# Performance work log

Hardware: AMD Instinct MI355X
Metric: run time of the kernel (lower is better)

## Reference

```python
import jax, jax.numpy as jnp
import numpy as np

D = 1024      # input_dim / embed_dim
H = 1024      # hidden_dim
H2 = H // 2
M = 15        # n_masks
NH = 4        # n_heads
B = 8192
LN_EPS = 1e-5


def setup_inputs() -> dict:
    key = jax.random.key(0)
    ks = jax.random.split(key, 16)
    s = 0.02
    return {
        "x": jax.random.normal(ks[0], (B, D), jnp.float32),
        # nn.MultiheadAttention params (torch layout: y = x @ W.T + b)
        "in_proj_w": jax.random.normal(ks[1], (3 * D, D), jnp.float32) * s,
        "in_proj_b": jax.random.normal(ks[2], (3 * D,), jnp.float32) * s,
        "out_proj_w": jax.random.normal(ks[3], (D, D), jnp.float32) * s,
        "out_proj_b": jax.random.normal(ks[4], (D,), jnp.float32) * s,
        # 15 mask MLPs stacked along leading axis (grouped GEMM form)
        "W1": jax.random.normal(ks[5], (M, D, H), jnp.float32) * s,
        "b1": jax.random.normal(ks[6], (M, H), jnp.float32) * s,
        "ln_g": jnp.ones((M, H), jnp.float32),
        "ln_b": jnp.zeros((M, H), jnp.float32),
        "W2": jax.random.normal(ks[7], (M, H, H2), jnp.float32) * s,
        "b2": jax.random.normal(ks[8], (M, H2), jnp.float32) * s,
        "W3": jax.random.normal(ks[9], (M, H2, D), jnp.float32) * s,
        "b3": jax.random.normal(ks[10], (M, D), jnp.float32) * s,
    }


def reference(x, in_proj_w, in_proj_b, out_proj_w, out_proj_b,
              W1, b1, ln_g, ln_b, W2, b2, W3, b3):
    Bn = x.shape[0]
    hd = D // NH
    # --- seq_len=1 self-attention ---
    qkv = x @ in_proj_w.T + in_proj_b                      # [B, 3D]
    q, k, v = jnp.split(qkv, 3, axis=-1)                   # each [B, D]
    qh = q.reshape(Bn, NH, hd)
    kh = k.reshape(Bn, NH, hd)
    vh = v.reshape(Bn, NH, hd)
    scores = jnp.sum(qh * kh, axis=-1) / jnp.sqrt(jnp.float32(hd))  # [B, NH]
    # softmax over kv length = 1 -> all ones (kept for faithfulness)
    w = jax.nn.softmax(scores[..., None], axis=-1)         # [B, NH, 1]
    attn = (w * vh).reshape(Bn, D)                         # [B, D]
    a = attn @ out_proj_w.T + out_proj_b                   # [B, D]
    # --- 15 mask MLPs as one grouped GEMM stack (Dropout is eval->identity) ---
    h1 = jnp.einsum('bd,mdh->mbh', a, W1) + b1[:, None, :]  # [M, B, H]
    mu = jnp.mean(h1, axis=-1, keepdims=True)
    var = jnp.mean(jnp.square(h1 - mu), axis=-1, keepdims=True)
    h1 = (h1 - mu) * jax.lax.rsqrt(var + LN_EPS) * ln_g[:, None, :] + ln_b[:, None, :]
    h1 = jax.nn.gelu(h1, approximate=False)
    h2 = jnp.einsum('mbh,mhk->mbk', h1, W2) + b2[:, None, :]  # [M, B, H2]
    h2 = jax.nn.gelu(h2, approximate=False)
    h3 = jnp.einsum('mbk,mkd->mbd', h2, W3) + b3[:, None, :]  # [M, B, D]
    return jax.nn.sigmoid(h3)                               # [M, B, D]
```

## Files before the change

### kernel.cpp

```cpp
#include <hip/hip_runtime.h>

#define D_  1024
#define H_  1024
#define H2_ 512
#define M_  15
#define B_  8192

typedef __attribute__((ext_vector_type(4))) float f32x4;
typedef __attribute__((ext_vector_type(8))) short short8;

__device__ __forceinline__ unsigned short f2bf(float f) {
  unsigned int u = __float_as_uint(f);
  u += 0x7fffu + ((u >> 16) & 1u);
  return (unsigned short)(u >> 16);
}
__device__ __forceinline__ float bf2f(unsigned int h) {
  return __uint_as_float(h << 16);
}
__device__ __forceinline__ float gelu_exact(float x) {
  return 0.5f * x * (1.0f + erff(x * 0.70710678118654752440f));
}

__global__ void cast_f32_bf16(const float* __restrict__ in, unsigned short* __restrict__ out, int n4) {
  int i = blockIdx.x * blockDim.x + threadIdx.x;
  if (i >= n4) return;
  float4 v = ((const float4*)in)[i];
  ushort4 o;
  o.x = f2bf(v.x); o.y = f2bf(v.y); o.z = f2bf(v.z); o.w = f2bf(v.w);
  ((ushort4*)out)[i] = o;
}

__global__ void transpose_cast(const float* __restrict__ in, unsigned short* __restrict__ out,
                               int K, int N) {
  __shared__ float t[32][33];
  const size_t mo = (size_t)blockIdx.z * K * N;
  in  += mo;
  out += mo;
  const int k0 = blockIdx.x * 32, n0 = blockIdx.y * 32;
  const int tx = threadIdx.x, ty = threadIdx.y;
#pragma unroll
  for (int j = 0; j < 32; j += 8)
    t[ty + j][tx] = in[(size_t)(k0 + ty + j) * N + (n0 + tx)];
  __syncthreads();
#pragma unroll
  for (int j = 0; j < 32; j += 8)
    out[(size_t)(n0 + ty + j) * K + (k0 + tx)] = f2bf(t[tx][ty + j]);
}

template <int EPI>
__launch_bounds__(256, 3)
__global__ void gemm_bt(const unsigned short* __restrict__ A, const unsigned short* __restrict__ Bt,
                        const float* __restrict__ bias, void* __restrict__ Cout,
                        int Mrows, int N, int K,
                        long sA, long sB, long sBias, long sC) {
  __shared__ __align__(16) unsigned short As[128 * 64];
  __shared__ __align__(16) unsigned short Bs[128 * 64];
  const int mz = blockIdx.z;
  A    += (size_t)mz * sA;
  Bt   += (size_t)mz * sB;
  bias += (size_t)mz * sBias;

  const int tid  = threadIdx.x;
  const int w    = tid >> 6;
  const int lane = tid & 63;
  const int row0 = blockIdx.x * 128;
  const int col0 = blockIdx.y * 128;

  f32x4 acc[4][4];
#pragma unroll
  for (int i = 0; i < 4; ++i)
#pragma unroll
    for (int j = 0; j < 4; ++j) acc[i][j] = (f32x4){0.f, 0.f, 0.f, 0.f};

  const int wm = w >> 1, wn = w & 1;
  const int mrow = lane & 15;
  const int kq   = (lane >> 4) << 3;

  for (int k0 = 0; k0 < K; k0 += 64) {
    __syncthreads();
#pragma unroll
    for (int i = 0; i < 4; ++i) {
      const int c  = i * 256 + tid;
      const int m  = c >> 3;
      const int kk = (c & 7) << 3;
      const unsigned short* gA = A  + (size_t)(row0 + m) * K + (k0 + kk);
      const unsigned short* gB = Bt + (size_t)(col0 + m) * K + (k0 + kk);
      const int ldsoff = (i * 256 + w * 64) * 8;
      __builtin_amdgcn_global_load_lds((const __attribute__((address_space(1))) void*)gA,
                                       (__attribute__((address_space(3))) void*)(As + ldsoff),
                                       16, 0, 0);
      __builtin_amdgcn_global_load_lds((const __attribute__((address_space(1))) void*)gB,
                                       (__attribute__((address_space(3))) void*)(Bs + ldsoff),
                                       16, 0, 0);
    }
    __syncthreads();
#pragma unroll
    for (int ki = 0; ki < 64; ki += 32) {
      short8 af[4], bf[4];
#pragma unroll
      for (int f = 0; f < 4; ++f) {
        af[f] = *(const short8*)(As + (wm * 64 + f * 16 + mrow) * 64 + ki + kq);
        bf[f] = *(const short8*)(Bs + (wn * 64 + f * 16 + mrow) * 64 + ki + kq);
      }
#pragma unroll
      for (int fm = 0; fm < 4; ++fm)
#pragma unroll
        for (int fn = 0; fn < 4; ++fn)
          acc[fm][fn] = __builtin_amdgcn_mfma_f32_16x16x32_bf16(af[fm], bf[fn], acc[fm][fn], 0, 0, 0);
    }
  }

  float*          Cf = (float*)Cout          + (size_t)mz * sC;
  unsigned short* Cb = (unsigned short*)Cout + (size_t)mz * sC;
  const int rq = (lane >> 4) << 2;
  const int cl = lane & 15;
#pragma unroll
  for (int fm = 0; fm < 4; ++fm) {
#pragma unroll
    for (int fn = 0; fn < 4; ++fn) {
      const int cc = col0 + wn * 64 + fn * 16 + cl;
      const float bv = bias[cc];
#pragma unroll
      for (int r = 0; r < 4; ++r) {
        const int rr = row0 + wm * 64 + fm * 16 + rq + r;
        float v = acc[fm][fn][r] + bv;
        if (EPI == 2) {
          Cf[(size_t)rr * N + cc] = 1.0f / (1.0f + __expf(-v));
        } else {
          if (EPI == 1) v = gelu_exact(v);
          Cb[(size_t)rr * N + cc] = f2bf(v);
        }
      }
    }
  }
}

#define BAR()   asm volatile("s_barrier" ::: "memory")
#define LGKM0() asm volatile("s_waitcnt lgkmcnt(0)" ::: "memory")
#define VM6()   asm volatile("s_waitcnt vmcnt(6)" ::: "memory")

#define STG_A(bufi, kt, rho0) do {                                                             \
  _Pragma("unroll")                                                                            \
  for (int j_ = 0; j_ < 2; ++j_) {                                                             \
    const int rho_ = (rho0) + j_ * 64 + (tid >> 3);                                            \
    const int gr_  = (((rho_ >> 6) & 1) << 7) | (((rho_ >> 7) & 1) << 6) | (rho_ & 63);        \
    const unsigned short* g_ = A + (size_t)(row0 + gr_) * K + (size_t)(kt) * 64                \
                                 + (((tid & 7) ^ (rho_ & 7)) << 3);                            \
    __builtin_amdgcn_global_load_lds((const __attribute__((address_space(1))) void*)g_,        \
        (__attribute__((address_space(3))) void*)(&As[bufi][(rho0) * 64 + (j_ * 512 + w6 * 64) * 8]), \
        16, 0, 0);                                                                             \
  }                                                                                            \
} while (0)

#define STG_B(bufi, kt, rho0) do {                                                             \
  _Pragma("unroll")                                                                            \
  for (int j_ = 0; j_ < 2; ++j_) {                                                             \
    const int rho_ = (rho0) + j_ * 64 + (tid >> 3);                                            \
    const int gc_  = (((rho_ >> 5) & 3) << 6) | (((rho_ >> 7) & 1) << 5) | (rho_ & 31);        \
    const unsigned short* g_ = Bt + (size_t)(col0 + gc_) * K + (size_t)(kt) * 64               \
                                  + (((tid & 7) ^ (rho_ & 7)) << 3);                           \
    __builtin_amdgcn_global_load_lds((const __attribute__((address_space(1))) void*)g_,        \
        (__attribute__((address_space(3))) void*)(&Bs[bufi][(rho0) * 64 + (j_ * 512 + w6 * 64) * 8]), \
        16, 0, 0);                                                                             \
  }                                                                                            \
} while (0)

#define LDA4(bufi, hi) do {                                                                    \
  _Pragma("unroll")                                                                            \
  for (int q_ = 0; q_ < 4; ++q_) {                                                             \
    const int rho_ = ((hi) ? 128 : 0) + wm * 64 + q_ * 16 + lrow;                              \
    a[q_][0] = *(const short8*)&As[bufi][rho_ * 64 + ((lk ^ (rho_ & 7)) << 3)];                \
    a[q_][1] = *(const short8*)&As[bufi][rho_ * 64 + (((4 + lk) ^ (rho_ & 7)) << 3)];          \
  }                                                                                            \
} while (0)

#define LDB2(bufi, hi) do {                                                                    \
  _Pragma("unroll")                                                                            \
  for (int q_ = 0; q_ < 2; ++q_) {                                                             \
    const int rho_ = ((hi) ? 128 : 0) + wn * 32 + q_ * 16 + lrow;                              \
    b[(hi) * 2 + q_][0] = *(const short8*)&Bs[bufi][rho_ * 64 + ((lk ^ (rho_ & 7)) << 3)];     \
    b[(hi) * 2 + q_][1] = *(const short8*)&Bs[bufi][rho_ * 64 + (((4 + lk) ^ (rho_ & 7)) << 3)]; \
  }                                                                                            \
} while (0)

#define MMQ(mh, nh) do {                                                                       \
  __builtin_amdgcn_s_setprio(1);                                                               \
  _Pragma("unroll")                                                                            \
  for (int mq_ = 0; mq_ < 4; ++mq_) {                                                          \
    _Pragma("unroll")                                                                          \
    for (int nq_ = 0; nq_ < 2; ++nq_) {                                                        \
      acc[(mh) * 4 + mq_][(nh) * 2 + nq_] = __builtin_amdgcn_mfma_f32_16x16x32_bf16(           \
          a[mq_][0], b[(nh) * 2 + nq_][0], acc[(mh) * 4 + mq_][(nh) * 2 + nq_], 0, 0, 0);      \
      acc[(mh) * 4 + mq_][(nh) * 2 + nq_] = __builtin_amdgcn_mfma_f32_16x16x32_bf16(           \
          a[mq_][1], b[(nh) * 2 + nq_][1], acc[(mh) * 4 + mq_][(nh) * 2 + nq_], 0, 0, 0);      \
    }                                                                                          \
  }                                                                                            \
  __builtin_amdgcn_s_setprio(0);                                                               \
} while (0)

template <int EPI>
__launch_bounds__(512, 2)
__global__ void gemm256(const unsigned short* __restrict__ A, const unsigned short* __restrict__ Bt,
                        const float* __restrict__ bias, void* __restrict__ Cout,
                        int N, int K, long sA, long sB, long sBias, long sC) {
  __shared__ __align__(16) unsigned short As[2][256 * 64];
  __shared__ __align__(16) unsigned short Bs[2][256 * 64];

  const int gx = gridDim.x, gy = gridDim.y;
  const int nwg = gx * gy * gridDim.z;
  const int bid = blockIdx.x + gx * (blockIdx.y + gy * blockIdx.z);
  int orig = bid;
  if ((nwg & 7) == 0) {
    const int cpx = nwg >> 3;
    orig = (bid & 7) * cpx + (bid >> 3);
  }
  const int bx = orig % gx;
  const int r1 = orig / gx;
  const int by = r1 % gy;
  const int mz = r1 / gy;

  A    += (size_t)mz * sA;
  Bt   += (size_t)mz * sB;
  bias += (size_t)mz * sBias;

  const int tid  = threadIdx.x;
  const int w6   = tid >> 6;
  const int lane = tid & 63;
  const int wm   = w6 >> 2;
  const int wn   = w6 & 3;
  const int lrow = lane & 15;
  const int lk   = lane >> 4;
  const int row0 = bx * 256;
  const int col0 = by * 256;
  const int nt   = K >> 6;

  f32x4 acc[8][4];
#pragma unroll
  for (int i = 0; i < 8; ++i)
#pragma unroll
    for (int j = 0; j < 4; ++j) acc[i][j] = (f32x4){0.f, 0.f, 0.f, 0.f};
  short8 a[4][2], b[4][2];

  STG_A(0, 0, 0); STG_B(0, 0, 0); STG_B(0, 0, 128); STG_A(0, 0, 128);
  STG_A(1, 1, 0); STG_B(1, 1, 0); STG_B(1, 1, 128);
  VM6(); BAR();

#pragma unroll 1
  for (int it = 0; it < (nt >> 1); ++it) {
    const int T  = it * 2;
    const int t2 = (T + 2 < nt) ? T + 2 : nt - 1;
    const int t3 = (T + 3 < nt) ? T + 3 : nt - 1;
    LDA4(0, 0); LDB2(0, 0);
    STG_A(1, T + 1, 128);
    BAR(); LGKM0();
    MMQ(0, 0);
    BAR();
    LDB2(0, 1);
    STG_A(0, t2, 0);
    BAR(); LGKM0();
    MMQ(0, 1);
    BAR();
    LDA4(0, 1);
    STG_B(0, t2, 0);
    BAR(); LGKM0();
    MMQ(1, 0);
    BAR();
    STG_B(0, t2, 128);
    VM6(); BAR();
    MMQ(1, 1);
    BAR();
    LDA4(1, 0); LDB2(1, 0);
    STG_A(0, t2, 128);
    BAR(); LGKM0();
    MMQ(0, 0);
    BAR();
    LDB2(1, 1);
    STG_A(1, t3, 0);
    BAR(); LGKM0();
    MMQ(0, 1);
    BAR();
    LDA4(1, 1);
    STG_B(1, t3, 0);
    BAR(); LGKM0();
    MMQ(1, 0);
    BAR();
    STG_B(1, t3, 128);
    VM6(); BAR();
    MMQ(1, 1);
    BAR();
  }
  asm volatile("s_waitcnt vmcnt(0)" ::: "memory");

  float*          Cf = (float*)Cout          + (size_t)mz * sC;
  unsigned short* Cb = (unsigned short*)Cout + (size_t)mz * sC;
  const int rq = (lane >> 4) << 2;
  const int cl = lane & 15;
#pragma unroll
  for (int nf = 0; nf < 4; ++nf) {
    const int cc = col0 + wn * 64 + nf * 16 + cl;
    const float bv = bias[cc];
#pragma unroll
    for (int mf = 0; mf < 8; ++mf) {
#pragma unroll
      for (int r = 0; r < 4; ++r) {
        const int rr = row0 + wm * 128 + mf * 16 + rq + r;
        float v = acc[mf][nf][r] + bv;
        if (EPI == 2) {
          Cf[(size_t)rr * N + cc] = 1.0f / (1.0f + __expf(-v));
        } else {
          if (EPI == 1) v = gelu_exact(v);
          Cb[(size_t)rr * N + cc] = f2bf(v);
        }
      }
    }
  }
}

__global__ void ln_gelu(const unsigned short* __restrict__ in, const float* __restrict__ g,
                        const float* __restrict__ bb, unsigned short* __restrict__ out) {
  const int m = blockIdx.y;
  in  += (size_t)m * B_ * H_;
  out += (size_t)m * B_ * H_;
  g   += (size_t)m * H_;
  bb  += (size_t)m * H_;
  const int row = blockIdx.x;
  const int tid = threadIdx.x;
  const unsigned short* rp = in + (size_t)row * H_;
  uint2 u = ((const uint2*)rp)[tid];
  float x0 = bf2f(u.x & 0xffffu);
  float x1 = bf2f(u.x >> 16);
  float x2 = bf2f(u.y & 0xffffu);
  float x3 = bf2f(u.y >> 16);

  float s  = x0 + x1 + x2 + x3;
  float s2 = x0 * x0 + x1 * x1 + x2 * x2 + x3 * x3;
#pragma unroll
  for (int o = 32; o > 0; o >>= 1) {
    s  += __shfl_down(s, o);
    s2 += __shfl_down(s2, o);
  }
  __shared__ float red[10];
  const int w = tid >> 6;
  if ((tid & 63) == 0) { red[w] = s; red[4 + w] = s2; }
  __syncthreads();
  if (tid == 0) {
    float ts = red[0] + red[1] + red[2] + red[3];
    float t2 = red[4] + red[5] + red[6] + red[7];
    float mean = ts * (1.0f / H_);
    float var  = t2 * (1.0f / H_) - mean * mean;
    red[8] = mean;
    red[9] = rsqrtf(var + 1e-5f);
  }
  __syncthreads();
  const float mean = red[8], rstd = red[9];
  const int col = tid * 4;
  float y0 = gelu_exact((x0 - mean) * rstd * g[col + 0] + bb[col + 0]);
  float y1 = gelu_exact((x1 - mean) * rstd * g[col + 1] + bb[col + 1]);
  float y2 = gelu_exact((x2 - mean) * rstd * g[col + 2] + bb[col + 2]);
  float y3 = gelu_exact((x3 - mean) * rstd * g[col + 3] + bb[col + 3]);
  ushort4 o;
  o.x = f2bf(y0); o.y = f2bf(y1); o.z = f2bf(y2); o.w = f2bf(y3);
  ((ushort4*)(out + (size_t)row * H_))[tid] = o;
}

extern "C" void kernel_launch(void* const* d_in, const int* in_sizes, int n_in,
                              void* d_out, int out_size, void* d_ws, size_t ws_size,
                              hipStream_t stream) {
  const float* x   = (const float*)d_in[0];
  const float* ipw = (const float*)d_in[1];
  const float* ipb = (const float*)d_in[2];
  const float* opw = (const float*)d_in[3];
  const float* opb = (const float*)d_in[4];
  const float* W1  = (const float*)d_in[5];
  const float* b1  = (const float*)d_in[6];
  const float* lng = (const float*)d_in[7];
  const float* lnb = (const float*)d_in[8];
  const float* W2  = (const float*)d_in[9];
  const float* b2  = (const float*)d_in[10];
  const float* W3  = (const float*)d_in[11];
  const float* b3  = (const float*)d_in[12];
  float* out = (float*)d_out;

  char* p = (char*)d_ws;
  auto take = [&](size_t bytes) { void* q = (void*)p; p += (bytes + 255) & ~(size_t)255; return q; };
  unsigned short* xb  = (unsigned short*)take((size_t)B_ * D_ * 2);
  unsigned short* wvb = (unsigned short*)take((size_t)D_ * D_ * 2);
  unsigned short* wob = (unsigned short*)take((size_t)D_ * D_ * 2);
  unsigned short* w1t = (unsigned short*)take((size_t)M_ * H_ * D_ * 2);
  unsigned short* w2t = (unsigned short*)take((size_t)M_ * H2_ * H_ * 2);
  unsigned short* w3t = (unsigned short*)take((size_t)M_ * D_ * H2_ * 2);
  unsigned short* vb  = (unsigned short*)take((size_t)B_ * D_ * 2);
  unsigned short* ab  = (unsigned short*)take((size_t)B_ * D_ * 2);
  unsigned short* h1p = (unsigned short*)take((size_t)M_ * B_ * H_ * 2);
  unsigned short* h1a = (unsigned short*)take((size_t)M_ * B_ * H_ * 2);
  unsigned short* h2b = (unsigned short*)take((size_t)M_ * B_ * H2_ * 2);

  cast_f32_bf16<<<dim3((B_ * D_ / 4 + 255) / 256), 256, 0, stream>>>(x, xb, B_ * D_ / 4);
  cast_f32_bf16<<<dim3((D_ * D_ / 4 + 255) / 256), 256, 0, stream>>>(ipw + 2 * D_ * D_, wvb, D_ * D_ / 4);
  cast_f32_bf16<<<dim3((D_ * D_ / 4 + 255) / 256), 256, 0, stream>>>(opw, wob, D_ * D_ / 4);
  transpose_cast<<<dim3(D_ / 32, H_ / 32, M_), dim3(32, 8), 0, stream>>>(W1, w1t, D_, H_);
  transpose_cast<<<dim3(H_ / 32, H2_ / 32, M_), dim3(32, 8), 0, stream>>>(W2, w2t, H_, H2_);
  transpose_cast<<<dim3(H2_ / 32, D_ / 32, M_), dim3(32, 8), 0, stream>>>(W3, w3t, H2_, D_);

  gemm_bt<0><<<dim3(B_ / 128, D_ / 128, 1), 256, 0, stream>>>(
      xb, wvb, ipb + 2 * D_, vb, B_, D_, D_, 0, 0, 0, 0);
  gemm_bt<0><<<dim3(B_ / 128, D_ / 128, 1), 256, 0, stream>>>(
      vb, wob, opb, ab, B_, D_, D_, 0, 0, 0, 0);

  gemm256<0><<<dim3(B_ / 256, H_ / 256, M_), 512, 0, stream>>>(
      ab, w1t, b1, h1p, H_, D_,
      0, (long)H_ * D_, (long)H_, (long)B_ * H_);
  ln_gelu<<<dim3(B_, M_), 256, 0, stream>>>(h1p, lng, lnb, h1a);
  gemm256<1><<<dim3(B_ / 256, H2_ / 256, M_), 512, 0, stream>>>(
      h1a, w2t, b2, h2b, H2_, H_,
      (long)B_ * H_, (long)H2_ * H_, (long)H2_, (long)B_ * H2_);
  gemm256<2><<<dim3(B_ / 256, D_ / 256, M_), 512, 0, stream>>>(
      h2b, w3t, b3, out, D_, H2_,
      (long)B_ * H2_, (long)D_ * H2_, (long)D_, (long)B_ * D_);
}
```

Baseline: 1.731 ms.

## Make grouped GEMMs persistent with cross-tile prefetch over a fixed grid

Replaces the per-tile launch of the three grouped MLP GEMMs with a persistent kernel of 240 workgroups. Each workgroup walks several output tiles in sequence, and the K-loop prefetch runs across tile boundaries, so loads for the next tile overlap the current tile's tail and epilogue. This is meant to remove the wave-quantization tail and the per-tile pipeline fill and drain. In exchange the epilogue now sits inside the main loop, which adds register pressure and per-iteration address arithmetic. The hard-coded tile stride of 30 and the XCD mapping depend on the grid size.

Result: faster. 1.623 ms (-6.2%).

```diff
diff --git a/kernel.cpp b/kernel.cpp
--- a/kernel.cpp
+++ b/kernel.cpp
@@ -139,26 +139,24 @@
 #define LGKM0() asm volatile("s_waitcnt lgkmcnt(0)" ::: "memory")
 #define VM6()   asm volatile("s_waitcnt vmcnt(6)" ::: "memory")
 
-#define STG_A(bufi, kt, rho0) do {                                                             \
+#define STG_A(bufi, bA, rho0) do {                                                             \
   _Pragma("unroll")                                                                            \
   for (int j_ = 0; j_ < 2; ++j_) {                                                             \
     const int rho_ = (rho0) + j_ * 64 + (tid >> 3);                                            \
     const int gr_  = (((rho_ >> 6) & 1) << 7) | (((rho_ >> 7) & 1) << 6) | (rho_ & 63);        \
-    const unsigned short* g_ = A + (size_t)(row0 + gr_) * K + (size_t)(kt) * 64                \
-                                 + (((tid & 7) ^ (rho_ & 7)) << 3);                            \
+    const unsigned short* g_ = (bA) + (size_t)gr_ * K + (((tid & 7) ^ (rho_ & 7)) << 3);       \
     __builtin_amdgcn_global_load_lds((const __attribute__((address_space(1))) void*)g_,        \
         (__attribute__((address_space(3))) void*)(&As[bufi][(rho0) * 64 + (j_ * 512 + w6 * 64) * 8]), \
         16, 0, 0);                                                                             \
   }                                                                                            \
 } while (0)
 
-#define STG_B(bufi, kt, rho0) do {                                                             \
+#define STG_B(bufi, bB, rho0) do {                                                             \
   _Pragma("unroll")                                                                            \
   for (int j_ = 0; j_ < 2; ++j_) {                                                             \
     const int rho_ = (rho0) + j_ * 64 + (tid >> 3);                                            \
     const int gc_  = (((rho_ >> 5) & 3) << 6) | (((rho_ >> 7) & 1) << 5) | (rho_ & 31);        \
-    const unsigned short* g_ = Bt + (size_t)(col0 + gc_) * K + (size_t)(kt) * 64               \
-                                  + (((tid & 7) ^ (rho_ & 7)) << 3);                           \
+    const unsigned short* g_ = (bB) + (size_t)gc_ * K + (((tid & 7) ^ (rho_ & 7)) << 3);       \
     __builtin_amdgcn_global_load_lds((const __attribute__((address_space(1))) void*)g_,        \
         (__attribute__((address_space(3))) void*)(&Bs[bufi][(rho0) * 64 + (j_ * 512 + w6 * 64) * 8]), \
         16, 0, 0);                                                                             \
@@ -198,30 +196,19 @@
   __builtin_amdgcn_s_setprio(0);                                                               \
 } while (0)
 
-template <int EPI>
+template <int EPI, int LNT, int LGY>
 __launch_bounds__(512, 2)
-__global__ void gemm256(const unsigned short* __restrict__ A, const unsigned short* __restrict__ Bt,
-                        const float* __restrict__ bias, void* __restrict__ Cout,
-                        int N, int K, long sA, long sB, long sBias, long sC) {
+__global__ void gemm256p(const unsigned short* __restrict__ A, const unsigned short* __restrict__ Bt,
+                         const float* __restrict__ bias, void* __restrict__ Cout,
+                         int N, int K, long sA, long sB, long sBias, long sC,
+                         int ntiles8, int tpb) {
   __shared__ __align__(16) unsigned short As[2][256 * 64];
   __shared__ __align__(16) unsigned short Bs[2][256 * 64];
-
-  const int gx = gridDim.x, gy = gridDim.y;
-  const int nwg = gx * gy * gridDim.z;
-  const int bid = blockIdx.x + gx * (blockIdx.y + gy * blockIdx.z);
-  int orig = bid;
-  if ((nwg & 7) == 0) {
-    const int cpx = nwg >> 3;
-    orig = (bid & 7) * cpx + (bid >> 3);
-  }
-  const int bx = orig % gx;
-  const int r1 = orig / gx;
-  const int by = r1 % gy;
-  const int mz = r1 / gy;
-
-  A    += (size_t)mz * sA;
-  Bt   += (size_t)mz * sB;
-  bias += (size_t)mz * sBias;
+  const int NT = 1 << LNT, GYm1 = (1 << LGY) - 1;
+
+  const int bid = blockIdx.x;
+  const int xcd = bid & 7, lb = bid >> 3;
+  const int cb  = xcd * ntiles8;
 
   const int tid  = threadIdx.x;
   const int w6   = tid >> 6;
@@ -230,9 +217,14 @@
   const int wn   = w6 & 3;
   const int lrow = lane & 15;
   const int lk   = lane >> 4;
-  const int row0 = bx * 256;
-  const int col0 = by * 256;
-  const int nt   = K >> 6;
+
+  int t_cur = 0;
+  int tix  = cb + lb;
+  int row0 = ((tix >> LGY) & 31) << 8;
+  int col0 = (tix & GYm1) << 8;
+  int mz   = tix >> (LGY + 5);
+  const unsigned short* bAc = A  + (size_t)mz * sA + (size_t)row0 * K;
+  const unsigned short* bBc = Bt + (size_t)mz * sB + (size_t)col0 * K;
 
   f32x4 acc[8][4];
 #pragma unroll
@@ -241,79 +233,92 @@
     for (int j = 0; j < 4; ++j) acc[i][j] = (f32x4){0.f, 0.f, 0.f, 0.f};
   short8 a[4][2], b[4][2];
 
-  STG_A(0, 0, 0); STG_B(0, 0, 0); STG_B(0, 0, 128); STG_A(0, 0, 128);
-  STG_A(1, 1, 0); STG_B(1, 1, 0); STG_B(1, 1, 128);
+  STG_A(0, bAc, 0); STG_B(0, bBc, 0); STG_B(0, bBc, 128); STG_A(0, bAc, 128);
+  STG_A(1, bAc + 64, 0); STG_B(1, bBc + 64, 0); STG_B(1, bBc + 64, 128);
   VM6(); BAR();
 
+  const int totK = tpb << LNT;
 #pragma unroll 1
-  for (int it = 0; it < (nt >> 1); ++it) {
-    const int T  = it * 2;
-    const int t2 = (T + 2 < nt) ? T + 2 : nt - 1;
-    const int t3 = (T + 3 < nt) ? T + 3 : nt - 1;
+  for (int T = 0; T < totK; T += 2) {
+    const int g2 = (T + 2 < totK) ? T + 2 : totK - 1;
+    const int g3 = (T + 3 < totK) ? T + 3 : totK - 1;
+    const int t2 = g2 >> LNT, t3 = g3 >> LNT;
+    const int tix2 = cb + lb + t2 * 30;
+    const int tix3 = cb + lb + t3 * 30;
+    const unsigned short* bA2 = A  + (size_t)(tix2 >> (LGY + 5)) * sA
+                                   + (size_t)((((tix2 >> LGY) & 31) << 8)) * K + ((g2 & (NT - 1)) << 6);
+    const unsigned short* bB2 = Bt + (size_t)(tix2 >> (LGY + 5)) * sB
+                                   + (size_t)(((tix2 & GYm1) << 8)) * K + ((g2 & (NT - 1)) << 6);
+    const unsigned short* bA3 = A  + (size_t)(tix3 >> (LGY + 5)) * sA
+                                   + (size_t)((((tix3 >> LGY) & 31) << 8)) * K + ((g3 & (NT - 1)) << 6);
+    const unsigned short* bB3 = Bt + (size_t)(tix3 >> (LGY + 5)) * sB
+                                   + (size_t)(((tix3 & GYm1) << 8)) * K + ((g3 & (NT - 1)) << 6);
+    const unsigned short* bA1 = bAc + (((T + 1) & (NT - 1)) << 6);
+
     LDA4(0, 0); LDB2(0, 0);
-    STG_A(1, T + 1, 128);
-    BAR(); LGKM0();
-    MMQ(0, 0);
-    BAR();
+    STG_A(1, bA1, 128);
+    BAR(); LGKM0(); MMQ(0, 0); BAR();
     LDB2(0, 1);
-    STG_A(0, t2, 0);
-    BAR(); LGKM0();
-    MMQ(0, 1);
-    BAR();
+    STG_A(0, bA2, 0);
+    BAR(); LGKM0(); MMQ(0, 1); BAR();
     LDA4(0, 1);
-    STG_B(0, t2, 0);
-    BAR(); LGKM0();
-    MMQ(1, 0);
-    BAR();
-    STG_B(0, t2, 128);
-    VM6(); BAR();
-    MMQ(1, 1);
-    BAR();
+    STG_B(0, bB2, 0);
+    BAR(); LGKM0(); MMQ(1, 0); BAR();
+    STG_B(0, bB2, 128);
+    VM6(); BAR(); MMQ(1, 1); BAR();
     LDA4(1, 0); LDB2(1, 0);
-    STG_A(0, t2, 128);
-    BAR(); LGKM0();
-    MMQ(0, 0);
-    BAR();
+    STG_A(0, bA2, 128);
+    BAR(); LGKM0(); MMQ(0, 0); BAR();
     LDB2(1, 1);
-    STG_A(1, t3, 0);
-    BAR(); LGKM0();
-    MMQ(0, 1);
-    BAR();
+    STG_A(1, bA3, 0);
+    BAR(); LGKM0(); MMQ(0, 1); BAR();
     LDA4(1, 1);
-    STG_B(1, t3, 0);
-    BAR(); LGKM0();
-    MMQ(1, 0);
-    BAR();
-    STG_B(1, t3, 128);
-    VM6(); BAR();
-    MMQ(1, 1);
-    BAR();
-  }
-  asm volatile("s_waitcnt vmcnt(0)" ::: "memory");
-
-  float*          Cf = (float*)Cout          + (size_t)mz * sC;
-  unsigned short* Cb = (unsigned short*)Cout + (size_t)mz * sC;
-  const int rq = (lane >> 4) << 2;
-  const int cl = lane & 15;
-#pragma unroll
-  for (int nf = 0; nf < 4; ++nf) {
-    const int cc = col0 + wn * 64 + nf * 16 + cl;
-    const float bv = bias[cc];
-#pragma unroll
-    for (int mf = 0; mf < 8; ++mf) {
-#pragma unroll
-      for (int r = 0; r < 4; ++r) {
-        const int rr = row0 + wm * 128 + mf * 16 + rq + r;
-        float v = acc[mf][nf][r] + bv;
-        if (EPI == 2) {
-          Cf[(size_t)rr * N + cc] = 1.0f / (1.0f + __expf(-v));
-        } else {
-          if (EPI == 1) v = gelu_exact(v);
-          Cb[(size_t)rr * N + cc] = f2bf(v);
+    STG_B(1, bB3, 0);
+    BAR(); LGKM0(); MMQ(1, 0); BAR();
+    STG_B(1, bB3, 128);
+    VM6(); BAR(); MMQ(1, 1); BAR();
+
+    if (((T + 2) & (NT - 1)) == 0) {
+      const float* bp = bias + (size_t)mz * sBias;
+      float*          Cf = (float*)Cout          + (size_t)mz * sC;
+      unsigned short* Cb = (unsigned short*)Cout + (size_t)mz * sC;
+      const int rq = (lane >> 4) << 2;
+      const int cl = lane & 15;
+#pragma unroll
+      for (int nf = 0; nf < 4; ++nf) {
+        const int cc = col0 + wn * 64 + nf * 16 + cl;
+        const float bv = bp[cc];
+#pragma unroll
+        for (int mf = 0; mf < 8; ++mf) {
+#pragma unroll
+          for (int r = 0; r < 4; ++r) {
+            const int rr = row0 + wm * 128 + mf * 16 + rq + r;
+            float v = acc[mf][nf][r] + bv;
+            if (EPI == 2) {
+              Cf[(size_t)rr * N + cc] = 1.0f / (1.0f + __expf(-v));
+            } else {
+              if (EPI == 1) v = gelu_exact(v);
+              Cb[(size_t)rr * N + cc] = f2bf(v);
+            }
+          }
         }
+      }
+#pragma unroll
+      for (int i = 0; i < 8; ++i)
+#pragma unroll
+        for (int j = 0; j < 4; ++j) acc[i][j] = (f32x4){0.f, 0.f, 0.f, 0.f};
+      ++t_cur;
+      if (t_cur < tpb) {
+        tix  = cb + lb + t_cur * 30;
+        row0 = ((tix >> LGY) & 31) << 8;
+        col0 = (tix & GYm1) << 8;
+        mz   = tix >> (LGY + 5);
+        bAc  = A  + (size_t)mz * sA + (size_t)row0 * K;
+        bBc  = Bt + (size_t)mz * sB + (size_t)col0 * K;
       }
     }
   }
+  asm volatile("s_waitcnt vmcnt(0)" ::: "memory");
 }
 
 __global__ void ln_gelu(const unsigned short* __restrict__ in, const float* __restrict__ g,
@@ -407,14 +412,14 @@
   gemm_bt<0><<<dim3(B_ / 128, D_ / 128, 1), 256, 0, stream>>>(
       vb, wob, opb, ab, B_, D_, D_, 0, 0, 0, 0);
 
-  gemm256<0><<<dim3(B_ / 256, H_ / 256, M_), 512, 0, stream>>>(
+  gemm256p<0, 4, 2><<<dim3(240), 512, 0, stream>>>(
       ab, w1t, b1, h1p, H_, D_,
-      0, (long)H_ * D_, (long)H_, (long)B_ * H_);
+      0, (long)H_ * D_, (long)H_, (long)B_ * H_, 1920 / 8, 8);
   ln_gelu<<<dim3(B_, M_), 256, 0, stream>>>(h1p, lng, lnb, h1a);
-  gemm256<1><<<dim3(B_ / 256, H2_ / 256, M_), 512, 0, stream>>>(
+  gemm256p<1, 4, 1><<<dim3(240), 512, 0, stream>>>(
       h1a, w2t, b2, h2b, H2_, H_,
-      (long)B_ * H_, (long)H2_ * H_, (long)H2_, (long)B_ * H2_);
-  gemm256<2><<<dim3(B_ / 256, D_ / 256, M_), 512, 0, stream>>>(
+      (long)B_ * H_, (long)H2_ * H_, (long)H2_, (long)B_ * H2_, 960 / 8, 4);
+  gemm256p<2, 3, 2><<<dim3(240), 512, 0, stream>>>(
       h2b, w3t, b3, out, D_, H2_,
-      (long)B_ * H2_, (long)D_ * H2_, (long)D_, (long)B_ * D_);
-}
+      (long)B_ * H2_, (long)D_ * H2_, (long)D_, (long)B_ * D_, 1920 / 8, 8);
+}
```
